# Performance work log

Measured on AMD Instinct MI355X. Metric: run time of the kernel, lower is better.

Reference implementation:

```python
import jax, jax.numpy as jnp
import numpy as np

EPS = 1e-6
TAU = 0.07


def setup_inputs() -> dict:
    key = jax.random.key(0)
    kx, ky = jax.random.split(key)
    B, D = 4096, 1024
    x = jax.random.normal(kx, (B, D), dtype=jnp.float32)
    y = jax.random.normal(ky, (B, D), dtype=jnp.float32)
    return {"x": x, "y": y}


def reference(x, y):
    B = x.shape[0]
    # torch CosineSimilarity: dot / (max(||x||, eps) * max(||y||, eps))
    xn = x / jnp.maximum(jnp.linalg.norm(x, axis=-1, keepdims=True), EPS)
    yn = y / jnp.maximum(jnp.linalg.norm(y, axis=-1, keepdims=True), EPS)
    S = jnp.einsum('id,jd->ij', xn, yn)          # [B, B] cosine sims, S[i,j]=cos(x_i,y_j)
    E = jnp.exp(S / TAU)                          # bounded: |S|<=1 so exp <= e^{1/0.07}
    diag = jnp.diagonal(E)
    # original: sum_j (exp + eps) + eps  ->  sum_j exp + B*eps + eps
    extra = B * EPS + EPS
    row_denom = jnp.sum(E, axis=1) + extra        # x->y direction (loop 1)
    col_denom = jnp.sum(E, axis=0) + extra        # y->x direction (loop 2)
    coef = -1.0 / (2.0 * B)
    loss = coef * (jnp.sum(jnp.log(diag / row_denom)) + jnp.sum(jnp.log(diag / col_denom)))
    return loss
```

## Files before the change

kernel.cpp:

```cpp
#include <hip/hip_runtime.h>
#include <hip/hip_bf16.h>

#define NB 4096
#define DK 1024
#define EPSF 1e-6f
#define QSCALE 16.0f

typedef __attribute__((ext_vector_type(8))) int   i32x8_t;
typedef __attribute__((ext_vector_type(4))) int   i32x4_t;
typedef __attribute__((ext_vector_type(4))) float f32x4_t;


__global__ __launch_bounds__(256) void normalize_rows(
    const float* __restrict__ x, const float* __restrict__ y,
    unsigned* __restrict__ xq, unsigned* __restrict__ yq,
    float* __restrict__ sdiag, float* __restrict__ zerobuf)
{
    const int t = threadIdx.x;
    const int gid = blockIdx.x * 256 + t;
    if (gid < 2 * NB) zerobuf[gid] = 0.f;

    const int wave = t >> 6;
    const int lane = t & 63;
    const int row  = blockIdx.x * 4 + wave;

    const float4* xr = reinterpret_cast<const float4*>(x + (size_t)row * DK);
    const float4* yr = reinterpret_cast<const float4*>(y + (size_t)row * DK);

    float4 xv[4], yv[4];
    float ssx = 0.f, ssy = 0.f, sxy = 0.f;
    #pragma unroll
    for (int j = 0; j < 4; ++j) {
        xv[j] = xr[j * 64 + lane];
        yv[j] = yr[j * 64 + lane];
        ssx += xv[j].x*xv[j].x + xv[j].y*xv[j].y + xv[j].z*xv[j].z + xv[j].w*xv[j].w;
        ssy += yv[j].x*yv[j].x + yv[j].y*yv[j].y + yv[j].z*yv[j].z + yv[j].w*yv[j].w;
        sxy += xv[j].x*yv[j].x + xv[j].y*yv[j].y + xv[j].z*yv[j].z + xv[j].w*yv[j].w;
    }
    #pragma unroll
    for (int off = 1; off < 64; off <<= 1) {
        ssx += __shfl_xor(ssx, off, 64);
        ssy += __shfl_xor(ssy, off, 64);
        sxy += __shfl_xor(sxy, off, 64);
    }
    const float invx = 1.0f / fmaxf(sqrtf(ssx), EPSF);
    const float invy = 1.0f / fmaxf(sqrtf(ssy), EPSF);
    const float sx = invx * QSCALE;
    const float sy = invy * QSCALE;

    const int p = row >> 4, r = row & 15;
    const int qs = (lane >> 3) & 3;
    const int bs = (lane & 7) * 4;
    #pragma unroll
    for (int j = 0; j < 4; ++j) {
        const int kb = j * 2 + (lane >> 5);
        const unsigned off = ((unsigned)(p * 32 + kb * 4 + qs) * 512 + r * 32 + bs) >> 2;
        int px = __builtin_amdgcn_cvt_pk_fp8_f32(xv[j].x * sx, xv[j].y * sx, 0, false);
        px     = __builtin_amdgcn_cvt_pk_fp8_f32(xv[j].z * sx, xv[j].w * sx, px, true);
        int py = __builtin_amdgcn_cvt_pk_fp8_f32(yv[j].x * sy, yv[j].y * sy, 0, false);
        py     = __builtin_amdgcn_cvt_pk_fp8_f32(yv[j].z * sy, yv[j].w * sy, py, true);
        xq[off] = (unsigned)px;
        yq[off] = (unsigned)py;
    }
    if (lane == 0) sdiag[row] = sxy * invx * invy;
}

__global__ __launch_bounds__(256) void gemm_exp_sums(
    const unsigned char* __restrict__ xq, const unsigned char* __restrict__ yq,
    float* __restrict__ rowsum, float* __restrict__ colsum)
{
    const int t    = threadIdx.x;
    const int lane = t & 63;
    const int wave = t >> 6;
    const int q    = lane >> 4;
    const int l15  = lane & 15;

    const int R0 = blockIdx.y * 128;
    const int C0 = blockIdx.x * 128;
    const int wRow = (wave >> 1) * 64;
    const int wCol = (wave & 1) * 64;

    f32x4_t acc[4][4];
    #pragma unroll
    for (int i = 0; i < 4; i++)
        #pragma unroll
        for (int j = 0; j < 4; j++)
            acc[i][j] = (f32x4_t){0.f, 0.f, 0.f, 0.f};

    const unsigned char* Abase =
        xq + (size_t)(((R0 + wRow) >> 4) * 32 + q) * 512 + l15 * 32;
    const unsigned char* Bbase =
        yq + (size_t)(((C0 + wCol) >> 4) * 32 + q) * 512 + l15 * 32;

    #pragma unroll 1
    for (int kb = 0; kb < 8; ++kb) {
        const unsigned char* Ak = Abase + kb * 2048;
        const unsigned char* Bk = Bbase + kb * 2048;

        i32x8_t bfr[4];
        #pragma unroll
        for (int nt = 0; nt < 4; ++nt) {
            const i32x4_t lo = *reinterpret_cast<const i32x4_t*>(Bk + nt * 16384);
            const i32x4_t hi = *reinterpret_cast<const i32x4_t*>(Bk + nt * 16384 + 16);
            bfr[nt][0] = lo[0]; bfr[nt][1] = lo[1]; bfr[nt][2] = lo[2]; bfr[nt][3] = lo[3];
            bfr[nt][4] = hi[0]; bfr[nt][5] = hi[1]; bfr[nt][6] = hi[2]; bfr[nt][7] = hi[3];
        }
        #pragma unroll
        for (int mt = 0; mt < 4; ++mt) {
            const i32x4_t lo = *reinterpret_cast<const i32x4_t*>(Ak + mt * 16384);
            const i32x4_t hi = *reinterpret_cast<const i32x4_t*>(Ak + mt * 16384 + 16);
            i32x8_t af;
            af[0] = lo[0]; af[1] = lo[1]; af[2] = lo[2]; af[3] = lo[3];
            af[4] = hi[0]; af[5] = hi[1]; af[6] = hi[2]; af[7] = hi[3];
            #pragma unroll
            for (int nt = 0; nt < 4; ++nt)
                acc[mt][nt] = __builtin_amdgcn_mfma_scale_f32_16x16x128_f8f6f4(
                    af, bfr[nt], acc[mt][nt],
                    0, 0,
                    0, 0x7F7F7F7F,
                    0, 0x7F7F7F7F);
        }
    }

    const float kScale = (float)(1.0 / (256.0 * 0.07 * 0.6931471805599453));
    float csum[4] = {0.f, 0.f, 0.f, 0.f};
    #pragma unroll
    for (int mt = 0; mt < 4; ++mt) {
        float rsum[4] = {0.f, 0.f, 0.f, 0.f};
        #pragma unroll
        for (int nt = 0; nt < 4; ++nt) {
            #pragma unroll
            for (int r = 0; r < 4; ++r) {
                const float e = exp2f(acc[mt][nt][r] * kScale);
                rsum[r]  += e;
                csum[nt] += e;
            }
        }
        #pragma unroll
        for (int r = 0; r < 4; ++r) {
            float v = rsum[r];
            v += __shfl_xor(v, 1, 64);
            v += __shfl_xor(v, 2, 64);
            v += __shfl_xor(v, 4, 64);
            v += __shfl_xor(v, 8, 64);
            if (l15 == 0)
                atomicAdd(&rowsum[R0 + wRow + mt * 16 + q * 4 + r], v);
        }
    }
    #pragma unroll
    for (int nt = 0; nt < 4; ++nt) {
        float v = csum[nt];
        v += __shfl_xor(v, 16, 64);
        v += __shfl_xor(v, 32, 64);
        if (lane < 16)
            atomicAdd(&colsum[C0 + wCol + nt * 16 + l15], v);
    }
}

__global__ __launch_bounds__(1024) void finalize(
    const float* __restrict__ rowsum, const float* __restrict__ colsum,
    const float* __restrict__ sdiag, float* __restrict__ out)
{
    const float extra = (float)(NB * 1e-6 + 1e-6);
    double local = 0.0;
    for (int i = threadIdx.x; i < NB; i += 1024) {
        local += (double)sdiag[i] * (2.0 / 0.07)
               - (double)logf(rowsum[i] + extra)
               - (double)logf(colsum[i] + extra);
    }
    #pragma unroll
    for (int off = 1; off < 64; off <<= 1)
        local += __shfl_xor(local, off, 64);
    __shared__ double dred[16];
    const int wave = threadIdx.x >> 6;
    if ((threadIdx.x & 63) == 0) dred[wave] = local;
    __syncthreads();
    if (threadIdx.x == 0) {
        double tot = 0.0;
        #pragma unroll
        for (int w = 0; w < 16; ++w) tot += dred[w];
        out[0] = (float)(tot * (-1.0 / (2.0 * NB)));
    }
}

extern "C" void kernel_launch(void* const* d_in, const int* in_sizes, int n_in,
                              void* d_out, int out_size, void* d_ws, size_t ws_size,
                              hipStream_t stream)
{
    const float* x = (const float*)d_in[0];
    const float* y = (const float*)d_in[1];
    float* out = (float*)d_out;

    char* ws = (char*)d_ws;
    unsigned char* xq = (unsigned char*)ws;
    unsigned char* yq = (unsigned char*)(ws + (size_t)4 * 1024 * 1024);
    float* rowsum = (float*)(ws + (size_t)8 * 1024 * 1024);
    float* colsum = rowsum + NB;
    float* sdiag  = colsum + NB;

    normalize_rows<<<NB / 4, 256, 0, stream>>>(x, y, (unsigned*)xq, (unsigned*)yq,
                                               sdiag, rowsum);

    dim3 grid(NB / 128, NB / 128);
    gemm_exp_sums<<<grid, 256, 0, stream>>>(xq, yq, rowsum, colsum);

    finalize<<<1, 1024, 0, stream>>>(rowsum, colsum, sdiag, out);
}
```

Baseline: 112.1 us.

## Software-pipeline B fragment loads and remap blocks across XCDs for L2 locality

```diff
diff --git a/kernel.cpp b/kernel.cpp
--- a/kernel.cpp
+++ b/kernel.cpp
@@ -65,6 +65,36 @@
     if (lane == 0) sdiag[row] = sxy * invx * invy;
 }
 
+__device__ __forceinline__ i32x8_t ldfrag(const unsigned char* p) {
+    const i32x4_t lo = *reinterpret_cast<const i32x4_t*>(p);
+    const i32x4_t hi = *reinterpret_cast<const i32x4_t*>(p + 16);
+    i32x8_t r;
+    r[0] = lo[0]; r[1] = lo[1]; r[2] = lo[2]; r[3] = lo[3];
+    r[4] = hi[0]; r[5] = hi[1]; r[6] = hi[2]; r[7] = hi[3];
+    return r;
+}
+
+__device__ __forceinline__ void stage(
+    const unsigned char* Abase, const unsigned char* Bbase,
+    int kb_cur, int kb_nxt,
+    i32x8_t (&bfC)[4], i32x8_t (&bfN)[4], f32x4_t (&acc)[4][4])
+{
+    #pragma unroll
+    for (int nt = 0; nt < 4; ++nt)
+        bfN[nt] = ldfrag(Bbase + kb_nxt * 2048 + nt * 16384);
+    #pragma unroll
+    for (int mt = 0; mt < 4; ++mt) {
+        const i32x8_t af = ldfrag(Abase + kb_cur * 2048 + mt * 16384);
+        #pragma unroll
+        for (int nt = 0; nt < 4; ++nt)
+            acc[mt][nt] = __builtin_amdgcn_mfma_scale_f32_16x16x128_f8f6f4(
+                af, bfC[nt], acc[mt][nt],
+                0, 0,
+                0, 0x7F7F7F7F,
+                0, 0x7F7F7F7F);
+    }
+}
+
 __global__ __launch_bounds__(256) void gemm_exp_sums(
     const unsigned char* __restrict__ xq, const unsigned char* __restrict__ yq,
     float* __restrict__ rowsum, float* __restrict__ colsum)
@@ -75,8 +105,14 @@
     const int q    = lane >> 4;
     const int l15  = lane & 15;
 
-    const int R0 = blockIdx.y * 128;
-    const int C0 = blockIdx.x * 128;
+    const int id  = blockIdx.x;
+    const int xcd = id & 7;
+    const int jj  = id >> 3;
+    const int by  = xcd * 4 + (jj >> 5);
+    const int bx  = jj & 31;
+
+    const int R0 = by * 128;
+    const int C0 = bx * 128;
     const int wRow = (wave >> 1) * 64;
     const int wCol = (wave & 1) * 64;
 
@@ -92,34 +128,15 @@
     const unsigned char* Bbase =
         yq + (size_t)(((C0 + wCol) >> 4) * 32 + q) * 512 + l15 * 32;
 
+    i32x8_t bf0[4], bf1[4];
+    #pragma unroll
+    for (int nt = 0; nt < 4; ++nt)
+        bf0[nt] = ldfrag(Bbase + nt * 16384);
+
     #pragma unroll 1
-    for (int kb = 0; kb < 8; ++kb) {
-        const unsigned char* Ak = Abase + kb * 2048;
-        const unsigned char* Bk = Bbase + kb * 2048;
-
-        i32x8_t bfr[4];
-        #pragma unroll
-        for (int nt = 0; nt < 4; ++nt) {
-            const i32x4_t lo = *reinterpret_cast<const i32x4_t*>(Bk + nt * 16384);
-            const i32x4_t hi = *reinterpret_cast<const i32x4_t*>(Bk + nt * 16384 + 16);
-            bfr[nt][0] = lo[0]; bfr[nt][1] = lo[1]; bfr[nt][2] = lo[2]; bfr[nt][3] = lo[3];
-            bfr[nt][4] = hi[0]; bfr[nt][5] = hi[1]; bfr[nt][6] = hi[2]; bfr[nt][7] = hi[3];
-        }
-        #pragma unroll
-        for (int mt = 0; mt < 4; ++mt) {
-            const i32x4_t lo = *reinterpret_cast<const i32x4_t*>(Ak + mt * 16384);
-            const i32x4_t hi = *reinterpret_cast<const i32x4_t*>(Ak + mt * 16384 + 16);
-            i32x8_t af;
-            af[0] = lo[0]; af[1] = lo[1]; af[2] = lo[2]; af[3] = lo[3];
-            af[4] = hi[0]; af[5] = hi[1]; af[6] = hi[2]; af[7] = hi[3];
-            #pragma unroll
-            for (int nt = 0; nt < 4; ++nt)
-                acc[mt][nt] = __builtin_amdgcn_mfma_scale_f32_16x16x128_f8f6f4(
-                    af, bfr[nt], acc[mt][nt],
-                    0, 0,
-                    0, 0x7F7F7F7F,
-                    0, 0x7F7F7F7F);
-        }
+    for (int kb = 0; kb < 8; kb += 2) {
+        stage(Abase, Bbase, kb,     kb + 1,       bf0, bf1, acc);
+        stage(Abase, Bbase, kb + 1, (kb + 2) & 7, bf1, bf0, acc);
     }
 
     const float kScale = (float)(1.0 / (256.0 * 0.07 * 0.6931471805599453));
@@ -201,8 +218,7 @@
     normalize_rows<<<NB / 4, 256, 0, stream>>>(x, y, (unsigned*)xq, (unsigned*)yq,
                                                sdiag, rowsum);
 
-    dim3 grid(NB / 128, NB / 128);
-    gemm_exp_sums<<<grid, 256, 0, stream>>>(xq, yq, rowsum, colsum);
+    gemm_exp_sums<<<1024, 256, 0, stream>>>(xq, yq, rowsum, colsum);
 
     finalize<<<1, 1024, 0, stream>>>(rowsum, colsum, sdiag, out);
 }
```

Result: slower. 117.8 us (+5.1%).

## Replace atomic row/column sum accumulation with per-block partial buffers

Applied to the files above, without the earlier changes.

```diff
diff --git a/kernel.cpp b/kernel.cpp
--- a/kernel.cpp
+++ b/kernel.cpp
@@ -14,12 +14,9 @@
 __global__ __launch_bounds__(256) void normalize_rows(
     const float* __restrict__ x, const float* __restrict__ y,
     unsigned* __restrict__ xq, unsigned* __restrict__ yq,
-    float* __restrict__ sdiag, float* __restrict__ zerobuf)
+    float* __restrict__ sdiag)
 {
     const int t = threadIdx.x;
-    const int gid = blockIdx.x * 256 + t;
-    if (gid < 2 * NB) zerobuf[gid] = 0.f;
-
     const int wave = t >> 6;
     const int lane = t & 63;
     const int row  = blockIdx.x * 4 + wave;
@@ -67,7 +64,7 @@
 
 __global__ __launch_bounds__(256) void gemm_exp_sums(
     const unsigned char* __restrict__ xq, const unsigned char* __restrict__ yq,
-    float* __restrict__ rowsum, float* __restrict__ colsum)
+    float* __restrict__ rowpart, float* __restrict__ colpart)
 {
     const int t    = threadIdx.x;
     const int lane = t & 63;
@@ -123,6 +120,9 @@
     }
 
     const float kScale = (float)(1.0 / (256.0 * 0.07 * 0.6931471805599453));
+    float* rowslot = rowpart + (size_t)(blockIdx.x * 2 + (wave & 1)) * NB;
+    float* colslot = colpart + (size_t)(blockIdx.y * 2 + (wave >> 1)) * NB;
+
     float csum[4] = {0.f, 0.f, 0.f, 0.f};
     #pragma unroll
     for (int mt = 0; mt < 4; ++mt) {
@@ -144,7 +144,7 @@
             v += __shfl_xor(v, 4, 64);
             v += __shfl_xor(v, 8, 64);
             if (l15 == 0)
-                atomicAdd(&rowsum[R0 + wRow + mt * 16 + q * 4 + r], v);
+                rowslot[R0 + wRow + mt * 16 + q * 4 + r] = v;
         }
     }
     #pragma unroll
@@ -153,20 +153,26 @@
         v += __shfl_xor(v, 16, 64);
         v += __shfl_xor(v, 32, 64);
         if (lane < 16)
-            atomicAdd(&colsum[C0 + wCol + nt * 16 + l15], v);
+            colslot[C0 + wCol + nt * 16 + l15] = v;
     }
 }
 
 __global__ __launch_bounds__(1024) void finalize(
-    const float* __restrict__ rowsum, const float* __restrict__ colsum,
+    const float* __restrict__ rowpart, const float* __restrict__ colpart,
     const float* __restrict__ sdiag, float* __restrict__ out)
 {
     const float extra = (float)(NB * 1e-6 + 1e-6);
     double local = 0.0;
     for (int i = threadIdx.x; i < NB; i += 1024) {
+        float rs = 0.f, cs = 0.f;
+        #pragma unroll 8
+        for (int s = 0; s < 64; ++s) {
+            rs += rowpart[s * NB + i];
+            cs += colpart[s * NB + i];
+        }
         local += (double)sdiag[i] * (2.0 / 0.07)
-               - (double)logf(rowsum[i] + extra)
-               - (double)logf(colsum[i] + extra);
+               - (double)logf(rs + extra)
+               - (double)logf(cs + extra);
     }
     #pragma unroll
     for (int off = 1; off < 64; off <<= 1)
@@ -194,15 +200,15 @@
     char* ws = (char*)d_ws;
     unsigned char* xq = (unsigned char*)ws;
     unsigned char* yq = (unsigned char*)(ws + (size_t)4 * 1024 * 1024);
-    float* rowsum = (float*)(ws + (size_t)8 * 1024 * 1024);
-    float* colsum = rowsum + NB;
-    float* sdiag  = colsum + NB;
+    float* rowpart = (float*)(ws + (size_t)8 * 1024 * 1024);
+    float* colpart = (float*)(ws + (size_t)9 * 1024 * 1024);
+    float* sdiag   = (float*)(ws + (size_t)10 * 1024 * 1024);
 
     normalize_rows<<<NB / 4, 256, 0, stream>>>(x, y, (unsigned*)xq, (unsigned*)yq,
-                                               sdiag, rowsum);
+                                               sdiag);
 
     dim3 grid(NB / 128, NB / 128);
-    gemm_exp_sums<<<grid, 256, 0, stream>>>(xq, yq, rowsum, colsum);
-
-    finalize<<<1, 1024, 0, stream>>>(rowsum, colsum, sdiag, out);
-}
+    gemm_exp_sums<<<grid, 256, 0, stream>>>(xq, yq, rowpart, colpart);
+
+    finalize<<<1, 1024, 0, stream>>>(rowpart, colpart, sdiag, out);
+}
```

After: 129.6 us. +15.6%, slower.

## Vectorize fp8 stores, stagger K order per wave, hoist all fragment loads

Applied to the files above, without the earlier changes.

```diff
diff --git a/kernel.cpp b/kernel.cpp
--- a/kernel.cpp
+++ b/kernel.cpp
@@ -13,7 +13,7 @@
 
 __global__ __launch_bounds__(256) void normalize_rows(
     const float* __restrict__ x, const float* __restrict__ y,
-    unsigned* __restrict__ xq, unsigned* __restrict__ yq,
+    unsigned char* __restrict__ xq, unsigned char* __restrict__ yq,
     float* __restrict__ sdiag, float* __restrict__ zerobuf)
 {
     const int t = threadIdx.x;
@@ -30,12 +30,12 @@
     float4 xv[4], yv[4];
     float ssx = 0.f, ssy = 0.f, sxy = 0.f;
     #pragma unroll
-    for (int j = 0; j < 4; ++j) {
-        xv[j] = xr[j * 64 + lane];
-        yv[j] = yr[j * 64 + lane];
-        ssx += xv[j].x*xv[j].x + xv[j].y*xv[j].y + xv[j].z*xv[j].z + xv[j].w*xv[j].w;
-        ssy += yv[j].x*yv[j].x + yv[j].y*yv[j].y + yv[j].z*yv[j].z + yv[j].w*yv[j].w;
-        sxy += xv[j].x*yv[j].x + xv[j].y*yv[j].y + xv[j].z*yv[j].z + xv[j].w*yv[j].w;
+    for (int jj = 0; jj < 4; ++jj) {
+        xv[jj] = xr[lane * 4 + jj];
+        yv[jj] = yr[lane * 4 + jj];
+        ssx += xv[jj].x*xv[jj].x + xv[jj].y*xv[jj].y + xv[jj].z*xv[jj].z + xv[jj].w*xv[jj].w;
+        ssy += yv[jj].x*yv[jj].x + yv[jj].y*yv[jj].y + yv[jj].z*yv[jj].z + yv[jj].w*yv[jj].w;
+        sxy += xv[jj].x*yv[jj].x + xv[jj].y*yv[jj].y + xv[jj].z*yv[jj].z + xv[jj].w*yv[jj].w;
     }
     #pragma unroll
     for (int off = 1; off < 64; off <<= 1) {
@@ -48,21 +48,33 @@
     const float sx = invx * QSCALE;
     const float sy = invy * QSCALE;
 
+    i32x4_t xb, yb;
+    #pragma unroll
+    for (int jj = 0; jj < 4; ++jj) {
+        int px = __builtin_amdgcn_cvt_pk_fp8_f32(xv[jj].x * sx, xv[jj].y * sx, 0, false);
+        px     = __builtin_amdgcn_cvt_pk_fp8_f32(xv[jj].z * sx, xv[jj].w * sx, px, true);
+        int py = __builtin_amdgcn_cvt_pk_fp8_f32(yv[jj].x * sy, yv[jj].y * sy, 0, false);
+        py     = __builtin_amdgcn_cvt_pk_fp8_f32(yv[jj].z * sy, yv[jj].w * sy, py, true);
+        xb[jj] = px;
+        yb[jj] = py;
+    }
+
     const int p = row >> 4, r = row & 15;
-    const int qs = (lane >> 3) & 3;
-    const int bs = (lane & 7) * 4;
-    #pragma unroll
-    for (int j = 0; j < 4; ++j) {
-        const int kb = j * 2 + (lane >> 5);
-        const unsigned off = ((unsigned)(p * 32 + kb * 4 + qs) * 512 + r * 32 + bs) >> 2;
-        int px = __builtin_amdgcn_cvt_pk_fp8_f32(xv[j].x * sx, xv[j].y * sx, 0, false);
-        px     = __builtin_amdgcn_cvt_pk_fp8_f32(xv[j].z * sx, xv[j].w * sx, px, true);
-        int py = __builtin_amdgcn_cvt_pk_fp8_f32(yv[j].x * sy, yv[j].y * sy, 0, false);
-        py     = __builtin_amdgcn_cvt_pk_fp8_f32(yv[j].z * sy, yv[j].w * sy, py, true);
-        xq[off] = (unsigned)px;
-        yq[off] = (unsigned)py;
-    }
+    const unsigned off = (unsigned)(p * 32 + (lane >> 3) * 4 + ((lane >> 1) & 3)) * 512
+                       + r * 32 + (lane & 1) * 16;
+    *reinterpret_cast<i32x4_t*>(xq + off) = xb;
+    *reinterpret_cast<i32x4_t*>(yq + off) = yb;
+
     if (lane == 0) sdiag[row] = sxy * invx * invy;
+}
+
+__device__ __forceinline__ i32x8_t ldfrag(const unsigned char* p) {
+    const i32x4_t lo = *reinterpret_cast<const i32x4_t*>(p);
+    const i32x4_t hi = *reinterpret_cast<const i32x4_t*>(p + 16);
+    i32x8_t r;
+    r[0] = lo[0]; r[1] = lo[1]; r[2] = lo[2]; r[3] = lo[3];
+    r[4] = hi[0]; r[5] = hi[1]; r[6] = hi[2]; r[7] = hi[3];
+    return r;
 }
 
 __global__ __launch_bounds__(256) void gemm_exp_sums(
@@ -92,34 +104,29 @@
     const unsigned char* Bbase =
         yq + (size_t)(((C0 + wCol) >> 4) * 32 + q) * 512 + l15 * 32;
 
+    const int kb0 = (2 * wave + (blockIdx.x & 1)) & 7;
+
     #pragma unroll 1
-    for (int kb = 0; kb < 8; ++kb) {
+    for (int s = 0; s < 8; ++s) {
+        const int kb = (kb0 + s) & 7;
         const unsigned char* Ak = Abase + kb * 2048;
         const unsigned char* Bk = Bbase + kb * 2048;
 
-        i32x8_t bfr[4];
-        #pragma unroll
-        for (int nt = 0; nt < 4; ++nt) {
-            const i32x4_t lo = *reinterpret_cast<const i32x4_t*>(Bk + nt * 16384);
-            const i32x4_t hi = *reinterpret_cast<const i32x4_t*>(Bk + nt * 16384 + 16);
-            bfr[nt][0] = lo[0]; bfr[nt][1] = lo[1]; bfr[nt][2] = lo[2]; bfr[nt][3] = lo[3];
-            bfr[nt][4] = hi[0]; bfr[nt][5] = hi[1]; bfr[nt][6] = hi[2]; bfr[nt][7] = hi[3];
-        }
-        #pragma unroll
-        for (int mt = 0; mt < 4; ++mt) {
-            const i32x4_t lo = *reinterpret_cast<const i32x4_t*>(Ak + mt * 16384);
-            const i32x4_t hi = *reinterpret_cast<const i32x4_t*>(Ak + mt * 16384 + 16);
-            i32x8_t af;
-            af[0] = lo[0]; af[1] = lo[1]; af[2] = lo[2]; af[3] = lo[3];
-            af[4] = hi[0]; af[5] = hi[1]; af[6] = hi[2]; af[7] = hi[3];
+        i32x8_t bfr[4], afr[4];
+        #pragma unroll
+        for (int nt = 0; nt < 4; ++nt) bfr[nt] = ldfrag(Bk + nt * 16384);
+        #pragma unroll
+        for (int mt = 0; mt < 4; ++mt) afr[mt] = ldfrag(Ak + mt * 16384);
+
+        #pragma unroll
+        for (int mt = 0; mt < 4; ++mt)
             #pragma unroll
             for (int nt = 0; nt < 4; ++nt)
                 acc[mt][nt] = __builtin_amdgcn_mfma_scale_f32_16x16x128_f8f6f4(
-                    af, bfr[nt], acc[mt][nt],
+                    afr[mt], bfr[nt], acc[mt][nt],
                     0, 0,
                     0, 0x7F7F7F7F,
                     0, 0x7F7F7F7F);
-        }
     }
 
     const float kScale = (float)(1.0 / (256.0 * 0.07 * 0.6931471805599453));
@@ -198,8 +205,7 @@
     float* colsum = rowsum + NB;
     float* sdiag  = colsum + NB;
 
-    normalize_rows<<<NB / 4, 256, 0, stream>>>(x, y, (unsigned*)xq, (unsigned*)yq,
-                                               sdiag, rowsum);
+    normalize_rows<<<NB / 4, 256, 0, stream>>>(x, y, xq, yq, sdiag, rowsum);
 
     dim3 grid(NB / 128, NB / 128);
     gemm_exp_sums<<<grid, 256, 0, stream>>>(xq, yq, rowsum, colsum);
```

After: 116.6 us. 1.04x slower.
